# Kernel tuning notes

Measured on AMD Instinct MI355X. Metric: run time of the kernel, lower is better.

## Reference

```python
import jax, jax.numpy as jnp
import numpy as np

D = 32        # dmodel (forced by reshape(..., 32) in the original)
N = 2000      # n_nodes == liner_fourth
SLOPE = 0.2   # LeakyReLU negative slope
EPS = 1e-6    # SublayerConnection LayerNorm eps (annotated-transformer style)


def _layernorm(x, g, b):
    m = x.mean(-1, keepdims=True)
    v = x.var(-1, keepdims=True)
    return g * (x - m) / jnp.sqrt(v + EPS) + b


def setup_inputs() -> dict:
    key = jax.random.key(0)
    ks = jax.random.split(key, 18)
    F_, NL, NS = 16, 500, 1500
    s = 0.1
    return {
        "state": jax.random.normal(ks[0], (F_, NS, D), jnp.float32),
        "left": jax.random.normal(ks[1], (F_, NL, D), jnp.float32),
        "inputad": jax.random.bernoulli(ks[2], 0.02, (F_, N, N)).astype(jnp.float32),
        "w3": s * jax.random.normal(ks[3], (D, D), jnp.float32),       # linearThird
        "b3": jnp.zeros((D,), jnp.float32),
        "attn_w": s * jax.random.normal(ks[4], (1, 2 * D), jnp.float32),  # attn (no bias)
        "w4": s * jax.random.normal(ks[5], (D, N), jnp.float32),       # linearFourth: 2000->32
        "b4": jnp.zeros((D,), jnp.float32),
        "w1": s * jax.random.normal(ks[6], (D, D), jnp.float32),       # linear
        "b1": jnp.zeros((D,), jnp.float32),
        "w_ih": s * jax.random.normal(ks[7], (4 * D, D), jnp.float32),  # LSTMCell (gate order i,f,g,o)
        "w_hh": s * jax.random.normal(ks[8], (4 * D, D), jnp.float32),
        "b_ih": jnp.zeros((4 * D,), jnp.float32),
        "b_hh": jnp.zeros((4 * D,), jnp.float32),
        "ln_g": jnp.ones((D,), jnp.float32),                            # SublayerConnection norm
        "ln_b": jnp.zeros((D,), jnp.float32),
        "w2": s * jax.random.normal(ks[9], (D, D), jnp.float32),        # linearSecond
        "b2": jnp.zeros((D,), jnp.float32),
    }


def reference(state, left, inputad, w3, b3, attn_w, w4, b4, w1, b1,
              w_ih, w_hh, b_ih, b_hh, ln_g, ln_b, w2, b2):
    # eval mode: all dropouts are identity
    x = jnp.concatenate([left, state], axis=1)          # [F, N, D]
    F_, n = x.shape[0], x.shape[1]
    g = x @ w3.T + b3                                   # [F, N, D]

    # torch: e = leaky(attn(cat([g.repeat_interleave(n,0), g.repeat(n,1,1)], -1)))
    # Decompose the linear over the concat: attn_w = [a_l | a_r].
    # g_repeat_interleave row m -> g[m // n]; g_repeat row m -> g[m % F_];
    # e.view(F_, n, n)[b, i, j] = e_flat[b*n + i, j].
    a_l, a_r = attn_w[0, :D], attn_w[0, D:]
    s_l = g @ a_l                                        # [F, N]
    s_r = g @ a_r                                        # [F, N]
    idx = (jnp.arange(F_)[:, None] * n + jnp.arange(n)[None, :]) % F_  # [F, N]
    e_mat = jax.nn.leaky_relu(s_l[:, None, :] + s_r[idx], SLOPE)       # [F, N, N]

    e_masked = jnp.where(inputad == 0, 0.0, e_mat)       # masked_fill(adj==0, 0)
    h = jax.nn.leaky_relu(jnp.einsum('bij,oj->bio', e_masked, w4) + b4, SLOPE)  # [F, N, 32]

    # first softmax(e)/dropout pair is dead code (overwritten); a = softmax(h, dim=1)
    a = jax.nn.softmax(h, axis=1)
    st = (a * g) @ w1.T + b1                             # elementwise branch (a.shape == g.shape)

    agg = jnp.matmul(inputad, st)                        # bmm(degree2, state): [F, N, D]

    # SublayerConnection: st + dropout(sublayer(norm(st))); sublayer = LSTMCell cell-state
    nx = _layernorm(st, ln_g, ln_b)
    c0 = nx.reshape(-1, D)                               # initial cell state = norm(st)
    # h0 = zeros, so the w_hh @ h0 contribution vanishes (b_hh still applies)
    gates = agg.reshape(-1, D) @ w_ih.T + b_ih + b_hh    # [F*N, 4D]
    i_g = jax.nn.sigmoid(gates[:, :D])
    f_g = jax.nn.sigmoid(gates[:, D:2 * D])
    g_g = jnp.tanh(gates[:, 2 * D:3 * D])
    c1 = f_g * c0 + i_g * g_g                            # LSTMCell returns (h', c'); [1] -> c'

    out = st + c1.reshape(F_, n, D)
    return out @ w2.T + b2
```

## Files before the change

### kernel.cpp

```cpp
#include <hip/hip_runtime.h>
#include <math.h>

#define F_    16
#define NROW  2000
#define NL    500
#define D     32
#define ROWS  (F_*NROW)
#define SLOPE 0.2f
#define CAP   128
#define LCAP  256

typedef float f4 __attribute__((ext_vector_type(4)));

__global__ __launch_bounds__(256) void k1_g(
    const float* __restrict__ state, const float* __restrict__ left,
    const float* __restrict__ w3, const float* __restrict__ b3,
    const float* __restrict__ attn_w, const float* __restrict__ w4,
    float* __restrict__ g, float* __restrict__ s_l, float* __restrict__ s_r,
    float* __restrict__ w4t)
{
    int bid = blockIdx.x;
    int t = threadIdx.x;
    if (bid >= ROWS/8) {
        int k = (bid - ROWS/8) * 256 + t;
        if (k < D * NROW) {
            int o = k / NROW, j = k - o * NROW;
            w4t[j * D + o] = w4[k];
        }
        return;
    }
    __shared__ float sw3[D*33];
    __shared__ float sb3[D], sal[D], sar[D];
    for (int k = t; k < D*D; k += 256) sw3[(k>>5)*33 + (k&31)] = w3[k];
    if (t < D) { sb3[t] = b3[t]; sal[t] = attn_w[t]; sar[t] = attn_w[D + t]; }
    __syncthreads();
    int grp = t >> 5, lane = t & 31;
    int row = bid * 8 + grp;
    int b = row / NROW, i = row - b * NROW;
    const float* xrow = (i < NL) ? (left  + ((size_t)b * NL + i) * D)
                                 : (state + ((size_t)b * (NROW - NL) + (i - NL)) * D);
    float x = xrow[lane];
    float acc = sb3[lane];
#pragma unroll
    for (int k = 0; k < D; ++k)
        acc += __shfl(x, k, 32) * sw3[lane*33 + k];
    g[(size_t)row * D + lane] = acc;
    float pl = acc * sal[lane], pr = acc * sar[lane];
#pragma unroll
    for (int m = 16; m >= 1; m >>= 1) {
        pl += __shfl_xor(pl, m, 32);
        pr += __shfl_xor(pr, m, 32);
    }
    if (lane == 0) { s_l[row] = pl; s_r[row] = pr; }
}

__global__ __launch_bounds__(256) void k2a_compact(
    const float* __restrict__ adj,
    int* __restrict__ nzc, unsigned short* __restrict__ nzi)
{
    __shared__ unsigned short sh_j[4][LCAP+8];
    int t = threadIdx.x;
    int w = t >> 6, lane = t & 63;
    int row = blockIdx.x * 4 + w;
    const f4* mrow = reinterpret_cast<const f4*>(adj + (size_t)row * NROW);

    f4 v[8];
#pragma unroll
    for (int it = 0; it < 7; ++it)
        v[it] = __builtin_nontemporal_load(mrow + it * 64 + lane);
    v[7] = (f4)(0.f);
    if (448 + lane < NROW/4) v[7] = __builtin_nontemporal_load(mrow + 448 + lane);

    int c = 0;
#pragma unroll
    for (int it = 0; it < 8; ++it)
        c += (v[it][0] != 0.f) + (v[it][1] != 0.f) + (v[it][2] != 0.f) + (v[it][3] != 0.f);
    int inc = c;
#pragma unroll
    for (int off = 1; off < 64; off <<= 1) {
        int n = __shfl_up(inc, off, 64);
        inc += (lane >= off) ? n : 0;
    }
    int pos = inc - c;
    int cnt = __shfl(inc, 63, 64);

#pragma unroll
    for (int it = 0; it < 8; ++it) {
        int jb = (it * 64 + lane) * 4;
#pragma unroll
        for (int cc = 0; cc < 4; ++cc) {
            float val = v[it][cc];
            int hit = (val != 0.f);
            int tgt = (hit && pos < LCAP) ? pos : LCAP;
            sh_j[w][tgt] = (unsigned short)(jb + cc);
            pos += hit;
        }
    }
    int cc2 = (cnt < CAP) ? cnt : CAP;
    for (int k = lane; k < cc2; k += 64)
        nzi[(size_t)row * CAP + k] = sh_j[w][k];
    if (lane == 0) nzc[row] = cc2;
}

__global__ __launch_bounds__(256) void k2b_h(
    const float* __restrict__ s_l, const float* __restrict__ s_r,
    const float* __restrict__ w4t, const float* __restrict__ b4,
    const int* __restrict__ nzc, const unsigned short* __restrict__ nzi,
    float* __restrict__ h)
{
    __shared__ float sh_e[8][CAP];
    __shared__ unsigned short sh_jj[8][CAP];
    int t = threadIdx.x;
    int grp = t >> 5, lane = t & 31;
    int row = blockIdx.x * 8 + grp;
    int b = row / NROW, i = row - b * NROW;
    int r = i & 15;
    int cnt = nzc[row];
    const unsigned short* lst = nzi + (size_t)row * CAP;
    const float* slb = s_l + (size_t)b * NROW;
    const float* srr = s_r + (size_t)r * NROW;
    for (int k = lane; k < cnt; k += 32) {
        int j = lst[k];
        sh_jj[grp][k] = (unsigned short)j;
        float e = slb[j] + srr[j];
        sh_e[grp][k] = (e > 0.f) ? e : SLOPE * e;
    }
    float acc = 0.f;
    int k = 0;
    for (; k + 4 <= cnt; k += 4) {
        int j0 = sh_jj[grp][k],   j1 = sh_jj[grp][k+1];
        int j2 = sh_jj[grp][k+2], j3 = sh_jj[grp][k+3];
        float w0 = w4t[j0*D + lane], w1 = w4t[j1*D + lane];
        float w2v = w4t[j2*D + lane], w3v = w4t[j3*D + lane];
        acc += sh_e[grp][k]   * w0 + sh_e[grp][k+1] * w1
             + sh_e[grp][k+2] * w2v + sh_e[grp][k+3] * w3v;
    }
    for (; k < cnt; ++k)
        acc += sh_e[grp][k] * w4t[sh_jj[grp][k]*D + lane];
    float hv = acc + b4[lane];
    h[(size_t)row * D + lane] = (hv > 0.f) ? hv : SLOPE * hv;
}

__global__ __launch_bounds__(256) void k3a_psum(const float* __restrict__ h,
                                                float* __restrict__ psum)
{
    int b = blockIdx.x, slice = blockIdx.y;
    int t = threadIdx.x;
    int o = t & 31, ti = t >> 5;
    int base = slice * 125;
    float s = 0.f;
    for (int i = base + ti; i < base + 125; i += 8)
        s += expf(h[((size_t)b * NROW + i) * D + o]);
    __shared__ float red[8][D];
    red[ti][o] = s;
    __syncthreads();
    if (t < D) {
        float tot = 0.f;
#pragma unroll
        for (int k = 0; k < 8; ++k) tot += red[k][t];
        psum[((size_t)b * 16 + slice) * D + t] = tot;
    }
}

__global__ __launch_bounds__(256) void k3b_st(
    const float* __restrict__ h, const float* __restrict__ g,
    const float* __restrict__ psum,
    const float* __restrict__ w1, const float* __restrict__ b1,
    float* __restrict__ st)
{
    __shared__ float sw1[D*33], sb1[D], ssum[D];
    int t = threadIdx.x;
    int bid = blockIdx.x;
    int b = bid / 250;
    for (int k = t; k < D*D; k += 256) sw1[(k>>5)*33 + (k&31)] = w1[k];
    if (t < D) {
        sb1[t] = b1[t];
        float tot = 0.f;
#pragma unroll
        for (int s = 0; s < 16; ++s) tot += psum[((size_t)b * 16 + s) * D + t];
        ssum[t] = tot;
    }
    __syncthreads();
    int grp = t >> 5, lane = t & 31;
    size_t row = (size_t)bid * 8 + grp;
    float p = (expf(h[row * D + lane]) / ssum[lane]) * g[row * D + lane];
    float acc = sb1[lane];
#pragma unroll
    for (int k = 0; k < D; ++k)
        acc += __shfl(p, k, 32) * sw1[lane*33 + k];
    st[row * D + lane] = acc;
}

__global__ __launch_bounds__(256) void k4_final(
    const float* __restrict__ st,
    const int* __restrict__ nzc, const unsigned short* __restrict__ nzi,
    const float* __restrict__ w_ih, const float* __restrict__ b_ih,
    const float* __restrict__ b_hh,
    const float* __restrict__ ln_g, const float* __restrict__ ln_b,
    const float* __restrict__ w2, const float* __restrict__ b2,
    float* __restrict__ out)
{
    __shared__ float swih[96*33];
    __shared__ float sw2[D*33];
    __shared__ float sbg[96];
    __shared__ float sb2[D], slg[D], slb[D];
    __shared__ unsigned short jl[8][CAP];
    __shared__ float aggsh[8][D];
    __shared__ float s2sh[8][D];

    int t = threadIdx.x;
    for (int k = t; k < 96*D; k += 256) swih[(k/D)*33 + (k%D)] = w_ih[k];
    for (int k = t; k < D*D;  k += 256) sw2 [(k/D)*33 + (k%D)] = w2[k];
    if (t < 96) sbg[t] = b_ih[t] + b_hh[t];
    if (t < D) { sb2[t] = b2[t]; slg[t] = ln_g[t]; slb[t] = ln_b[t]; }

    int grp = t >> 5, lane = t & 31;
    int row = blockIdx.x * 8 + grp;
    int b = row / NROW;
    int cnt = nzc[row];
    const unsigned short* lst = nzi + (size_t)row * CAP;
    for (int k = lane; k < cnt; k += 32) jl[grp][k] = lst[k];
    __syncthreads();

    const float* stb = st + (size_t)b * NROW * D;
    float agg = 0.f;
    int k = 0;
    for (; k + 8 <= cnt; k += 8) {
        int j0 = jl[grp][k],   j1 = jl[grp][k+1], j2 = jl[grp][k+2], j3 = jl[grp][k+3];
        int j4 = jl[grp][k+4], j5 = jl[grp][k+5], j6 = jl[grp][k+6], j7 = jl[grp][k+7];
        float a0 = stb[j0*D + lane], a1 = stb[j1*D + lane];
        float a2 = stb[j2*D + lane], a3 = stb[j3*D + lane];
        float a4 = stb[j4*D + lane], a5 = stb[j5*D + lane];
        float a6 = stb[j6*D + lane], a7 = stb[j7*D + lane];
        agg += ((a0 + a1) + (a2 + a3)) + ((a4 + a5) + (a6 + a7));
    }
    for (; k < cnt; ++k) agg += stb[jl[grp][k]*D + lane];

    float sv = st[(size_t)row * D + lane];

    float sum = sv;
#pragma unroll
    for (int m = 16; m >= 1; m >>= 1) sum += __shfl_xor(sum, m, 32);
    float mean = sum * (1.f / D);
    float dd = sv - mean;
    float vs = dd * dd;
#pragma unroll
    for (int m = 16; m >= 1; m >>= 1) vs += __shfl_xor(vs, m, 32);
    float inv = 1.f / sqrtf(vs * (1.f / D) + 1e-6f);
    float nx = slg[lane] * dd * inv + slb[lane];

    aggsh[grp][lane] = agg;

    float gi = sbg[lane], gf = sbg[lane + 32], gg = sbg[lane + 64];
#pragma unroll
    for (int d = 0; d < D; ++d) {
        float a = aggsh[grp][d];
        gi += swih[lane*33 + d]      * a;
        gf += swih[(lane+32)*33 + d] * a;
        gg += swih[(lane+64)*33 + d] * a;
    }
    float ig  = 1.f / (1.f + expf(-gi));
    float fg  = 1.f / (1.f + expf(-gf));
    float g_g = tanhf(gg);
    float s2  = sv + fg * nx + ig * g_g;

    s2sh[grp][lane] = s2;

    float acc = sb2[lane];
#pragma unroll
    for (int q = 0; q < D; ++q) acc += sw2[lane*33 + q] * s2sh[grp][q];
    out[(size_t)row * D + lane] = acc;
}

extern "C" void kernel_launch(void* const* d_in, const int* in_sizes, int n_in,
                              void* d_out, int out_size, void* d_ws, size_t ws_size,
                              hipStream_t stream)
{
    const float* state  = (const float*)d_in[0];
    const float* left   = (const float*)d_in[1];
    const float* adj    = (const float*)d_in[2];
    const float* w3     = (const float*)d_in[3];
    const float* b3     = (const float*)d_in[4];
    const float* attn_w = (const float*)d_in[5];
    const float* w4     = (const float*)d_in[6];
    const float* b4     = (const float*)d_in[7];
    const float* w1     = (const float*)d_in[8];
    const float* b1     = (const float*)d_in[9];
    const float* w_ih   = (const float*)d_in[10];
    const float* b_ih   = (const float*)d_in[12];
    const float* b_hh   = (const float*)d_in[13];
    const float* ln_g   = (const float*)d_in[14];
    const float* ln_b   = (const float*)d_in[15];
    const float* w2     = (const float*)d_in[16];
    const float* b2     = (const float*)d_in[17];
    float* out = (float*)d_out;

    float* g    = (float*)d_ws;
    float* h    = g  + (size_t)ROWS * D;
    float* st   = h  + (size_t)ROWS * D;
    float* s_l  = st + (size_t)ROWS * D;
    float* s_r  = s_l + ROWS;
    float* w4t  = s_r + ROWS;
    float* psum = w4t + (size_t)NROW * D;
    int*   nzc  = (int*)(psum + F_ * 16 * D);
    unsigned short* nzi = (unsigned short*)(nzc + ROWS);

    k1_g    <<<dim3(ROWS/8 + (D*NROW+255)/256), dim3(256), 0, stream>>>(
                state, left, w3, b3, attn_w, w4, g, s_l, s_r, w4t);
    k2a_compact<<<dim3(ROWS/4), dim3(256), 0, stream>>>(adj, nzc, nzi);
    k2b_h   <<<dim3(ROWS/8),  dim3(256), 0, stream>>>(s_l, s_r, w4t, b4, nzc, nzi, h);
    k3a_psum<<<dim3(F_, 16),  dim3(256), 0, stream>>>(h, psum);
    k3b_st  <<<dim3(ROWS/8),  dim3(256), 0, stream>>>(h, g, psum, w1, b1, st);
    k4_final<<<dim3(ROWS/8),  dim3(256), 0, stream>>>(st, nzc, nzi, w_ih, b_ih, b_hh,
                                                      ln_g, ln_b, w2, b2, out);
}
```

Baseline: 132.8 us.

## Merge g and adjacency-compaction kernels; fuse softmax column sums into h kernel via atomics

Combines the g/attention-score kernel, the w4 transpose and the adjacency compaction into one launch, and folds the per-batch exp column-sum into the h kernel with atomicAdd into a memset-zeroed psum. This removes two kernel launches and the separate pass that re-read h to compute the softmax denominators. In exchange it adds a memset and many atomics per batch column. It also drops the nontemporal loads on the adjacency stream and makes the float summation order nondeterministic.

```diff
diff --git a/kernel.cpp b/kernel.cpp
--- a/kernel.cpp
+++ b/kernel.cpp
@@ -12,104 +12,101 @@
 
 typedef float f4 __attribute__((ext_vector_type(4)));
 
-__global__ __launch_bounds__(256) void k1_g(
+struct KA_k1 { float sw3[D*33]; float sb3[D]; float sal[D]; float sar[D]; };
+union  KA_sm { int shj[4][LCAP+1]; KA_k1 k1; };
+
+__global__ __launch_bounds__(256) void kA(
+    const float* __restrict__ adj,
     const float* __restrict__ state, const float* __restrict__ left,
     const float* __restrict__ w3, const float* __restrict__ b3,
     const float* __restrict__ attn_w, const float* __restrict__ w4,
     float* __restrict__ g, float* __restrict__ s_l, float* __restrict__ s_r,
-    float* __restrict__ w4t)
-{
+    float* __restrict__ w4t, int* __restrict__ nzc, unsigned short* __restrict__ nzi)
+{
+    __shared__ KA_sm sm;
     int bid = blockIdx.x;
     int t = threadIdx.x;
-    if (bid >= ROWS/8) {
-        int k = (bid - ROWS/8) * 256 + t;
-        if (k < D * NROW) {
-            int o = k / NROW, j = k - o * NROW;
-            w4t[j * D + o] = w4[k];
+
+    if (bid < ROWS/4) {
+        int w = t >> 6, lane = t & 63;
+        int row = bid * 4 + w;
+        const f4* mrow = reinterpret_cast<const f4*>(adj + (size_t)row * NROW);
+        f4 v[8];
+#pragma unroll
+        for (int it = 0; it < 7; ++it)
+            v[it] = mrow[it * 64 + lane];
+        v[7] = (f4)(0.f);
+        if (448 + lane < NROW/4) v[7] = mrow[448 + lane];
+
+        int c = 0;
+#pragma unroll
+        for (int it = 0; it < 8; ++it)
+            c += (v[it][0] != 0.f) + (v[it][1] != 0.f) + (v[it][2] != 0.f) + (v[it][3] != 0.f);
+        int inc = c;
+#pragma unroll
+        for (int off = 1; off < 64; off <<= 1) {
+            int n = __shfl_up(inc, off, 64);
+            inc += (lane >= off) ? n : 0;
         }
+        int pos = inc - c;
+        int cnt = __shfl(inc, 63, 64);
+#pragma unroll
+        for (int it = 0; it < 8; ++it) {
+            int jb = (it * 64 + lane) * 4;
+#pragma unroll
+            for (int cc = 0; cc < 4; ++cc) {
+                int hit = (v[it][cc] != 0.f);
+                int tgt = (hit && pos < LCAP) ? pos : LCAP;
+                sm.shj[w][tgt] = jb + cc;
+                pos += hit;
+            }
+        }
+        int cc2 = (cnt < CAP) ? cnt : CAP;
+        for (int k = lane; k < cc2; k += 64)
+            nzi[(size_t)row * CAP + k] = (unsigned short)sm.shj[w][k];
+        if (lane == 0) nzc[row] = cc2;
         return;
     }
-    __shared__ float sw3[D*33];
-    __shared__ float sb3[D], sal[D], sar[D];
-    for (int k = t; k < D*D; k += 256) sw3[(k>>5)*33 + (k&31)] = w3[k];
-    if (t < D) { sb3[t] = b3[t]; sal[t] = attn_w[t]; sar[t] = attn_w[D + t]; }
-    __syncthreads();
-    int grp = t >> 5, lane = t & 31;
-    int row = bid * 8 + grp;
-    int b = row / NROW, i = row - b * NROW;
-    const float* xrow = (i < NL) ? (left  + ((size_t)b * NL + i) * D)
-                                 : (state + ((size_t)b * (NROW - NL) + (i - NL)) * D);
-    float x = xrow[lane];
-    float acc = sb3[lane];
-#pragma unroll
-    for (int k = 0; k < D; ++k)
-        acc += __shfl(x, k, 32) * sw3[lane*33 + k];
-    g[(size_t)row * D + lane] = acc;
-    float pl = acc * sal[lane], pr = acc * sar[lane];
-#pragma unroll
-    for (int m = 16; m >= 1; m >>= 1) {
-        pl += __shfl_xor(pl, m, 32);
-        pr += __shfl_xor(pr, m, 32);
-    }
-    if (lane == 0) { s_l[row] = pl; s_r[row] = pr; }
-}
-
-__global__ __launch_bounds__(256) void k2a_compact(
-    const float* __restrict__ adj,
-    int* __restrict__ nzc, unsigned short* __restrict__ nzi)
-{
-    __shared__ unsigned short sh_j[4][LCAP+8];
-    int t = threadIdx.x;
-    int w = t >> 6, lane = t & 63;
-    int row = blockIdx.x * 4 + w;
-    const f4* mrow = reinterpret_cast<const f4*>(adj + (size_t)row * NROW);
-
-    f4 v[8];
-#pragma unroll
-    for (int it = 0; it < 7; ++it)
-        v[it] = __builtin_nontemporal_load(mrow + it * 64 + lane);
-    v[7] = (f4)(0.f);
-    if (448 + lane < NROW/4) v[7] = __builtin_nontemporal_load(mrow + 448 + lane);
-
-    int c = 0;
-#pragma unroll
-    for (int it = 0; it < 8; ++it)
-        c += (v[it][0] != 0.f) + (v[it][1] != 0.f) + (v[it][2] != 0.f) + (v[it][3] != 0.f);
-    int inc = c;
-#pragma unroll
-    for (int off = 1; off < 64; off <<= 1) {
-        int n = __shfl_up(inc, off, 64);
-        inc += (lane >= off) ? n : 0;
-    }
-    int pos = inc - c;
-    int cnt = __shfl(inc, 63, 64);
-
-#pragma unroll
-    for (int it = 0; it < 8; ++it) {
-        int jb = (it * 64 + lane) * 4;
-#pragma unroll
-        for (int cc = 0; cc < 4; ++cc) {
-            float val = v[it][cc];
-            int hit = (val != 0.f);
-            int tgt = (hit && pos < LCAP) ? pos : LCAP;
-            sh_j[w][tgt] = (unsigned short)(jb + cc);
-            pos += hit;
+    if (bid < ROWS/4 + ROWS/8) {
+        for (int k = t; k < D*D; k += 256) sm.k1.sw3[(k>>5)*33 + (k&31)] = w3[k];
+        if (t < D) { sm.k1.sb3[t] = b3[t]; sm.k1.sal[t] = attn_w[t]; sm.k1.sar[t] = attn_w[D+t]; }
+        __syncthreads();
+        int grp = t >> 5, lane = t & 31;
+        int row = (bid - ROWS/4) * 8 + grp;
+        int b = row / NROW, i = row - b * NROW;
+        const float* xrow = (i < NL) ? (left  + ((size_t)b * NL + i) * D)
+                                     : (state + ((size_t)b * (NROW - NL) + (i - NL)) * D);
+        float x = xrow[lane];
+        float acc = sm.k1.sb3[lane];
+#pragma unroll
+        for (int k = 0; k < D; ++k)
+            acc += __shfl(x, k, 32) * sm.k1.sw3[lane*33 + k];
+        g[(size_t)row * D + lane] = acc;
+        float pl = acc * sm.k1.sal[lane], pr = acc * sm.k1.sar[lane];
+#pragma unroll
+        for (int m = 16; m >= 1; m >>= 1) {
+            pl += __shfl_xor(pl, m, 32);
+            pr += __shfl_xor(pr, m, 32);
         }
-    }
-    int cc2 = (cnt < CAP) ? cnt : CAP;
-    for (int k = lane; k < cc2; k += 64)
-        nzi[(size_t)row * CAP + k] = sh_j[w][k];
-    if (lane == 0) nzc[row] = cc2;
-}
-
-__global__ __launch_bounds__(256) void k2b_h(
+        if (lane == 0) { s_l[row] = pl; s_r[row] = pr; }
+        return;
+    }
+    int k = (bid - (ROWS/4 + ROWS/8)) * 256 + t;
+    if (k < D * NROW) {
+        int o = k / NROW, j = k - o * NROW;
+        w4t[j * D + o] = w4[k];
+    }
+}
+
+__global__ __launch_bounds__(256) void kB_h(
     const float* __restrict__ s_l, const float* __restrict__ s_r,
     const float* __restrict__ w4t, const float* __restrict__ b4,
     const int* __restrict__ nzc, const unsigned short* __restrict__ nzi,
-    float* __restrict__ h)
+    float* __restrict__ h, float* __restrict__ psum)
 {
     __shared__ float sh_e[8][CAP];
     __shared__ unsigned short sh_jj[8][CAP];
+    __shared__ float red[8][D];
     int t = threadIdx.x;
     int grp = t >> 5, lane = t & 31;
     int row = blockIdx.x * 8 + grp;
@@ -130,39 +127,25 @@
     for (; k + 4 <= cnt; k += 4) {
         int j0 = sh_jj[grp][k],   j1 = sh_jj[grp][k+1];
         int j2 = sh_jj[grp][k+2], j3 = sh_jj[grp][k+3];
-        float w0 = w4t[j0*D + lane], w1 = w4t[j1*D + lane];
-        float w2v = w4t[j2*D + lane], w3v = w4t[j3*D + lane];
-        acc += sh_e[grp][k]   * w0 + sh_e[grp][k+1] * w1
-             + sh_e[grp][k+2] * w2v + sh_e[grp][k+3] * w3v;
+        acc += sh_e[grp][k]   * w4t[j0*D + lane] + sh_e[grp][k+1] * w4t[j1*D + lane]
+             + sh_e[grp][k+2] * w4t[j2*D + lane] + sh_e[grp][k+3] * w4t[j3*D + lane];
     }
     for (; k < cnt; ++k)
         acc += sh_e[grp][k] * w4t[sh_jj[grp][k]*D + lane];
     float hv = acc + b4[lane];
-    h[(size_t)row * D + lane] = (hv > 0.f) ? hv : SLOPE * hv;
-}
-
-__global__ __launch_bounds__(256) void k3a_psum(const float* __restrict__ h,
-                                                float* __restrict__ psum)
-{
-    int b = blockIdx.x, slice = blockIdx.y;
-    int t = threadIdx.x;
-    int o = t & 31, ti = t >> 5;
-    int base = slice * 125;
-    float s = 0.f;
-    for (int i = base + ti; i < base + 125; i += 8)
-        s += expf(h[((size_t)b * NROW + i) * D + o]);
-    __shared__ float red[8][D];
-    red[ti][o] = s;
+    hv = (hv > 0.f) ? hv : SLOPE * hv;
+    h[(size_t)row * D + lane] = hv;
+    red[grp][lane] = expf(hv);
     __syncthreads();
     if (t < D) {
         float tot = 0.f;
 #pragma unroll
-        for (int k = 0; k < 8; ++k) tot += red[k][t];
-        psum[((size_t)b * 16 + slice) * D + t] = tot;
-    }
-}
-
-__global__ __launch_bounds__(256) void k3b_st(
+        for (int kk = 0; kk < 8; ++kk) tot += red[kk][t];
+        atomicAdd(&psum[b * D + t], tot);
+    }
+}
+
+__global__ __launch_bounds__(256) void kC_st(
     const float* __restrict__ h, const float* __restrict__ g,
     const float* __restrict__ psum,
     const float* __restrict__ w1, const float* __restrict__ b1,
@@ -173,13 +156,7 @@
     int bid = blockIdx.x;
     int b = bid / 250;
     for (int k = t; k < D*D; k += 256) sw1[(k>>5)*33 + (k&31)] = w1[k];
-    if (t < D) {
-        sb1[t] = b1[t];
-        float tot = 0.f;
-#pragma unroll
-        for (int s = 0; s < 16; ++s) tot += psum[((size_t)b * 16 + s) * D + t];
-        ssum[t] = tot;
-    }
+    if (t < D) { sb1[t] = b1[t]; ssum[t] = psum[b * D + t]; }
     __syncthreads();
     int grp = t >> 5, lane = t & 31;
     size_t row = (size_t)bid * 8 + grp;
@@ -191,7 +168,7 @@
     st[row * D + lane] = acc;
 }
 
-__global__ __launch_bounds__(256) void k4_final(
+__global__ __launch_bounds__(256) void kD_final(
     const float* __restrict__ st,
     const int* __restrict__ nzc, const unsigned short* __restrict__ nzi,
     const float* __restrict__ w_ih, const float* __restrict__ b_ih,
@@ -302,15 +279,16 @@
     float* s_r  = s_l + ROWS;
     float* w4t  = s_r + ROWS;
     float* psum = w4t + (size_t)NROW * D;
-    int*   nzc  = (int*)(psum + F_ * 16 * D);
+    int*   nzc  = (int*)(psum + F_ * D);
     unsigned short* nzi = (unsigned short*)(nzc + ROWS);
 
-    k1_g    <<<dim3(ROWS/8 + (D*NROW+255)/256), dim3(256), 0, stream>>>(
-                state, left, w3, b3, attn_w, w4, g, s_l, s_r, w4t);
-    k2a_compact<<<dim3(ROWS/4), dim3(256), 0, stream>>>(adj, nzc, nzi);
-    k2b_h   <<<dim3(ROWS/8),  dim3(256), 0, stream>>>(s_l, s_r, w4t, b4, nzc, nzi, h);
-    k3a_psum<<<dim3(F_, 16),  dim3(256), 0, stream>>>(h, psum);
-    k3b_st  <<<dim3(ROWS/8),  dim3(256), 0, stream>>>(h, g, psum, w1, b1, st);
-    k4_final<<<dim3(ROWS/8),  dim3(256), 0, stream>>>(st, nzc, nzi, w_ih, b_ih, b_hh,
-                                                      ln_g, ln_b, w2, b2, out);
-}
+    hipMemsetAsync(psum, 0, F_ * D * sizeof(float), stream);
+
+    int nA = ROWS/4 + ROWS/8 + (D*NROW + 255)/256;
+    kA      <<<dim3(nA),     dim3(256), 0, stream>>>(adj, state, left, w3, b3,
+                 attn_w, w4, g, s_l, s_r, w4t, nzc, nzi);
+    kB_h    <<<dim3(ROWS/8), dim3(256), 0, stream>>>(s_l, s_r, w4t, b4, nzc, nzi, h, psum);
+    kC_st   <<<dim3(ROWS/8), dim3(256), 0, stream>>>(h, g, psum, w1, b1, st);
+    kD_final<<<dim3(ROWS/8), dim3(256), 0, stream>>>(st, nzc, nzi, w_ih, b_ih, b_hh,
+                 ln_g, ln_b, w2, b2, out);
+}
```

New measurement: 133.1 us. No clear change (+0.3%).
